# Optimization experiments

Measured on AMD Instinct MI355X. Metric: run time of the kernel, lower is better.

Reference implementation:

```python
import jax, jax.numpy as jnp
import numpy as np

B, D, N, M, H = 2, 256, 4096, 4096, 4
DIM = D // H          # per-head dim = 64
D8 = D // 8           # bottleneck = 32
TD = 2 * D            # concat channels = 512
TD8 = TD // 8         # mlp bottleneck = 64
BN_EPS = 1e-5


def _pw(x, W, b):
    # Conv1d kernel_size=1 == pointwise matmul over channel dim. x: [B,Cin,N]
    return jnp.einsum('oi,bin->bon', W, x) + b[None, :, None]


def setup_inputs() -> dict:
    key = jax.random.key(0)
    ks = jax.random.split(key, 32)
    s = 0.05
    p = lambda i, shape: jax.random.normal(ks[i], shape, dtype=jnp.float32) * s
    inp = {
        'x': jax.random.normal(ks[0], (B, D, N), dtype=jnp.float32),
        'source': jax.random.normal(ks[1], (B, D, M), dtype=jnp.float32),
        # proj[0] (query): Conv(D->D/8) then Conv(D/8->D)
        'Wq1': p(2, (D8, D)), 'bq1': p(3, (D8,)), 'Wq2': p(4, (D, D8)), 'bq2': p(5, (D,)),
        # proj[1] (key)
        'Wk1': p(6, (D8, D)), 'bk1': p(7, (D8,)), 'Wk2': p(8, (D, D8)), 'bk2': p(9, (D,)),
        # proj[2] (value)
        'Wv1': p(10, (D8, D)), 'bv1': p(11, (D8,)), 'Wv2': p(12, (D, D8)), 'bv2': p(13, (D,)),
        # merge
        'Wm1': p(14, (D8, D)), 'bm1': p(15, (D8,)), 'Wm2': p(16, (D, D8)), 'bm2': p(17, (D,)),
        # mlp: Conv(2D->2D/8), BN(gamma,beta), ReLU, Conv(2D/8->D) with zero-init bias
        'Wp1': p(18, (TD8, TD)), 'bp1': p(19, (TD8,)),
        'g1': jnp.ones((TD8,), dtype=jnp.float32) + p(20, (TD8,)),
        'be1': p(21, (TD8,)),
        'Wp2': p(22, (D, TD8)), 'bp2': jnp.zeros((D,), dtype=jnp.float32),
    }
    return inp


def reference(x, source, Wq1, bq1, Wq2, bq2, Wk1, bk1, Wk2, bk2, Wv1, bv1, Wv2, bv2,
              Wm1, bm1, Wm2, bm2, Wp1, bp1, g1, be1, Wp2, bp2):
    # bottleneck projections, then split channels into (per-head dim, heads)
    q = _pw(_pw(x, Wq1, bq1), Wq2, bq2).reshape(B, DIM, H, N)
    k = _pw(_pw(source, Wk1, bk1), Wk2, bk2).reshape(B, DIM, H, M)
    v = _pw(_pw(source, Wv1, bv1), Wv2, bv2).reshape(B, DIM, H, M)
    scores = jnp.einsum('bdhn,bdhm->bhnm', q, k) / jnp.sqrt(jnp.float32(DIM))
    prob = jax.nn.softmax(scores, axis=-1)          # [B,H,N,M] -- the big one
    msg = jnp.einsum('bhnm,bdhm->bdhn', prob, v).reshape(B, D, N)
    msg = _pw(_pw(msg, Wm1, bm1), Wm2, bm2)          # merge
    h = _pw(jnp.concatenate([x, msg], axis=1), Wp1, bp1)
    # BatchNorm1d in eval mode with running_mean=0, running_var=1
    h = jax.nn.relu(g1[None, :, None] * h / jnp.sqrt(1.0 + BN_EPS) + be1[None, :, None])
    return _pw(h, Wp2, bp2)
```

## Files before the change

kernel.cpp:

```cpp
#include <hip/hip_runtime.h>
#include <hip/hip_bf16.h>

typedef unsigned short ushort_t;
typedef unsigned int uint_t;

constexpr int Bb = 2, Dd = 256, Nn = 4096, Mm = 4096, Hh = 4;
constexpr int NSPLIT = 2;
constexpr int MCHUNK = Mm / NSPLIT;
constexpr int NT = MCHUNK / 64;
constexpr int BH = Bb * Hh;

typedef __attribute__((ext_vector_type(8))) short bf16x8;
typedef __attribute__((ext_vector_type(4))) float f32x4;

__device__ __forceinline__ ushort_t f2b(float f) {
    union { float f; uint_t u; } v; v.f = f;
    uint_t u = v.u;
    uint_t r = u + 0x7FFFu + ((u >> 16) & 1u);
    return (ushort_t)(r >> 16);
}

__device__ __forceinline__ int swz(int row, int ch, int rowlen, int keymask) {
    return row * rowlen + (((ch >> 3) ^ (row & keymask)) << 3) + (ch & 7);
}

__device__ __forceinline__ f32x4 MF(bf16x8 a, bf16x8 b, f32x4 c) {
    return __builtin_amdgcn_mfma_f32_16x16x32_bf16(a, b, c, 0, 0, 0);
}

#define BARRIER() do { __builtin_amdgcn_sched_barrier(0); __builtin_amdgcn_s_barrier(); __builtin_amdgcn_sched_barrier(0); } while (0)

__global__ __launch_bounds__(256) void cvt_weights(
    const float* __restrict__ Wq1, const float* __restrict__ Wq2,
    const float* __restrict__ Wk1, const float* __restrict__ Wk2,
    const float* __restrict__ Wv1, const float* __restrict__ Wv2,
    const float* __restrict__ Wm1, const float* __restrict__ Wm2,
    const float* __restrict__ Wp1, const float* __restrict__ Wp2,
    ushort_t* __restrict__ WB)
{
    const int i = blockIdx.x * 256 + threadIdx.x;
    const float* src; int off, n;
    switch (blockIdx.y) {
        case 0: src = Wq1; off = 0;     n = 8192;  break;
        case 1: src = Wq2; off = 8192;  n = 8192;  break;
        case 2: src = Wk1; off = 16384; n = 8192;  break;
        case 3: src = Wk2; off = 24576; n = 8192;  break;
        case 4: src = Wv1; off = 32768; n = 8192;  break;
        case 5: src = Wv2; off = 40960; n = 8192;  break;
        case 6: src = Wm1; off = 49152; n = 8192;  break;
        case 7: src = Wm2; off = 57344; n = 8192;  break;
        case 8: src = Wp1; off = 65536; n = 32768; break;
        default: src = Wp2; off = 98304; n = 16384; break;
    }
    if (i < n) WB[off + i] = f2b(src[i]);
}

__global__ __launch_bounds__(256) void proj_mfma(
    const float* __restrict__ x, const float* __restrict__ source,
    const ushort_t* __restrict__ WB,
    const float* __restrict__ bq1, const float* __restrict__ bq2,
    const float* __restrict__ bk1, const float* __restrict__ bk2,
    const float* __restrict__ bv1, const float* __restrict__ bv2,
    ushort_t* __restrict__ Qb, ushort_t* __restrict__ Kb, ushort_t* __restrict__ Vt)
{
    __shared__ __align__(16) ushort_t Xs[16 * 256];
    __shared__ __align__(16) ushort_t t1T[16 * 32];

    const int which = blockIdx.y;
    const float* X = (which == 0) ? x : source;
    const ushort_t* W1b = WB + which * 16384;
    const ushort_t* W2b = W1b + 8192;
    const float* b1 = (which == 0) ? bq1 : (which == 1) ? bk1 : bv1;
    const float* b2 = (which == 0) ? bq2 : (which == 1) ? bk2 : bv2;
    const float oscale = (which == 0) ? 0.125f * 1.44269504f : 1.0f;

    const int t = threadIdx.x;
    const int bpb = Nn / 16;
    const int b = blockIdx.x / bpb;
    const int n0 = (blockIdx.x % bpb) * 16;
    const int wave = t >> 6, lane = t & 63;
    const int r16 = lane & 15, q4 = lane >> 4;

    #pragma unroll
    for (int i = 0; i < 16; ++i) {
        int idx = t + i * 256;
        int c = idx >> 4, col = idx & 15;
        Xs[swz(col, c, 256, 7)] = f2b(X[(size_t)(b * Dd + c) * Nn + n0 + col]);
    }
    __syncthreads();

    if (wave < 2) {
        const int arow = wave * 16 + r16;
        const ushort_t* wrow = W1b + arow * 256;
        f32x4 acc = (f32x4){0.f, 0.f, 0.f, 0.f};
        #pragma unroll
        for (int kc = 0; kc < 8; ++kc) {
            bf16x8 af = *(const bf16x8*)(wrow + kc * 32 + q4 * 8);
            bf16x8 bfr = *(const bf16x8*)&Xs[swz(r16, kc * 32 + q4 * 8, 256, 7)];
            acc = MF(af, bfr, acc);
        }
        const int chb = wave * 16 + q4 * 4;
        ushort4 pk;
        pk.x = f2b(acc[0] + b1[chb + 0]);
        pk.y = f2b(acc[1] + b1[chb + 1]);
        pk.z = f2b(acc[2] + b1[chb + 2]);
        pk.w = f2b(acc[3] + b1[chb + 3]);
        *(ushort4*)&t1T[swz(r16, chb, 32, 3)] = pk;
    }
    __syncthreads();

    const bf16x8 bmid = *(const bf16x8*)&t1T[swz(r16, q4 * 8, 32, 3)];
    #pragma unroll
    for (int i = 0; i < 4; ++i) {
        const int rt = wave * 4 + i;
        const int arow = rt * 16 + r16;
        bf16x8 af = *(const bf16x8*)(W2b + arow * 32 + q4 * 8);
        f32x4 acc = MF(af, bmid, (f32x4){0.f, 0.f, 0.f, 0.f});
        const int chb = rt * 16 + q4 * 4;
        const int d = chb >> 2;
        if (which == 2) {
            #pragma unroll
            for (int r = 0; r < 4; ++r)
                Vt[(((size_t)(b * Hh + r)) * 64 + d) * (size_t)Nn + n0 + r16] =
                    f2b(acc[r] + b2[chb + r]);
        } else {
            ushort_t* O = (which == 0) ? Qb : Kb;
            #pragma unroll
            for (int r = 0; r < 4; ++r)
                O[(((size_t)(b * Hh + r)) * Nn + n0 + r16) * 64 + d] =
                    f2b((acc[r] + b2[chb + r]) * oscale);
        }
    }
}

__global__ __launch_bounds__(256, 4) void attn_kernel(
    const ushort_t* __restrict__ Qb, const ushort_t* __restrict__ Kb,
    const ushort_t* __restrict__ Vt,
    float* __restrict__ PO, float* __restrict__ PL)
{
    __shared__ __align__(16) ushort_t kvbuf[2][8192];
    __shared__ __align__(16) ushort_t plds[4][1024];

    const int bid0 = blockIdx.x;
    const int orig = (bid0 & 7) * 128 + (bid0 >> 3);
    const int nt_ = orig & 63;
    const int chunk = orig >> 6;
    const int sp = chunk & (NSPLIT - 1);
    const int bh = chunk >> 1;
    const int n0 = nt_ * 64;
    const int mbase = sp * MCHUNK;

    const int t = threadIdx.x;
    const int wave = t >> 6, lane = t & 63;
    const int r16 = lane & 15, q4 = lane >> 4;
    const int sw = r16 & 7;

    const ushort_t* qp = Qb + (((size_t)bh * Nn) + n0 + wave * 16 + r16) * 64 + q4 * 8;
    const bf16x8 aq0 = *(const bf16x8*)qp;
    const bf16x8 aq1 = *(const bf16x8*)(qp + 32);

    f32x4 accO[4];
    float lsum[4];
    #pragma unroll
    for (int i = 0; i < 4; ++i) { accO[i] = (f32x4){0.f, 0.f, 0.f, 0.f}; lsum[i] = 0.f; }

    const ushort_t* Ktile0 = Kb + ((size_t)bh * Mm + mbase) * 64;
    const ushort_t* Vrow0  = Vt + ((size_t)bh * 64) * (size_t)Mm + mbase;

    auto stage = [&](int buf, int kt) {
        const ushort_t* ks = Ktile0 + (size_t)kt * 64 * 64;
        const ushort_t* vs = Vrow0 + kt * 64;
        ushort_t* kb = &kvbuf[buf][0];
        ushort_t* vb = &kvbuf[buf][4096];
        #pragma unroll
        for (int p = 0; p < 2; ++p) {
            int c = p * 256 + t;
            int row = c >> 3, gs = (c & 7) ^ (row & 7);
            __builtin_amdgcn_global_load_lds((const uint_t*)(ks + row * 64 + gs * 8),
                                             (uint_t*)(kb + c * 8), 16, 0, 0);
        }
        #pragma unroll
        for (int p = 0; p < 2; ++p) {
            int c = p * 256 + t;
            int row = c >> 3, gs = (c & 7) ^ (row & 7);
            __builtin_amdgcn_global_load_lds((const uint_t*)(vs + (size_t)row * Mm + gs * 8),
                                             (uint_t*)(vb + c * 8), 16, 0, 0);
        }
    };

    stage(0, 0);
    int cur = 0;

    for (int kt = 0; kt < NT; ++kt) {
        if (kt + 1 < NT) {
            stage(cur ^ 1, kt + 1);
            asm volatile("s_waitcnt vmcnt(4)" ::: "memory");
        } else {
            asm volatile("s_waitcnt vmcnt(0)" ::: "memory");
        }
        BARRIER();

        const ushort_t* kb = &kvbuf[cur][0];
        const ushort_t* vb = &kvbuf[cur][4096];

        f32x4 s[4];
        #pragma unroll
        for (int mt = 0; mt < 4; ++mt) {
            int row = mt * 16 + r16;
            bf16x8 bk0 = *(const bf16x8*)(kb + row * 64 + ((q4 ^ sw) * 8));
            bf16x8 bk1 = *(const bf16x8*)(kb + row * 64 + (((q4 + 4) ^ sw) * 8));
            f32x4 a = (f32x4){0.f, 0.f, 0.f, 0.f};
            a = MF(aq0, bk0, a);
            a = MF(aq1, bk1, a);
            s[mt] = a;
        }

        ushort_t* pw = &plds[wave][0];
        #pragma unroll
        for (int r = 0; r < 4; ++r) {
            int prow = q4 * 4 + r;
            int rsw = prow & 7;
            #pragma unroll
            for (int mt = 0; mt < 4; ++mt) {
                float p = exp2f(s[mt][r]);
                lsum[r] += p;
                int pcol = mt * 16 + r16;
                pw[prow * 64 + (((pcol >> 3) ^ rsw) * 8) + (pcol & 7)] = f2b(p);
            }
        }
        bf16x8 ap0 = *(const bf16x8*)(pw + r16 * 64 + ((q4 ^ sw) * 8));
        bf16x8 ap1 = *(const bf16x8*)(pw + r16 * 64 + (((q4 + 4) ^ sw) * 8));

        #pragma unroll
        for (int dt = 0; dt < 4; ++dt) {
            int row = dt * 16 + r16;
            bf16x8 bv0 = *(const bf16x8*)(vb + row * 64 + ((q4 ^ sw) * 8));
            bf16x8 bv1 = *(const bf16x8*)(vb + row * 64 + (((q4 + 4) ^ sw) * 8));
            accO[dt] = MF(ap0, bv0, accO[dt]);
            accO[dt] = MF(ap1, bv1, accO[dt]);
        }
        BARRIER();
        cur ^= 1;
    }

    const size_t pobase = ((size_t)sp * BH + bh) * Nn;
    #pragma unroll
    for (int r = 0; r < 4; ++r) {
        float rs = lsum[r];
        rs += __shfl_xor(rs, 1);
        rs += __shfl_xor(rs, 2);
        rs += __shfl_xor(rs, 4);
        rs += __shfl_xor(rs, 8);
        lsum[r] = rs;
    }
    #pragma unroll
    for (int dt = 0; dt < 4; ++dt) {
        #pragma unroll
        for (int r = 0; r < 4; ++r) {
            int n = n0 + wave * 16 + q4 * 4 + r;
            PO[(pobase + n) * 64 + dt * 16 + r16] = accO[dt][r];
        }
    }
    if (r16 == 0) {
        #pragma unroll
        for (int r = 0; r < 4; ++r) {
            int n = n0 + wave * 16 + q4 * 4 + r;
            PL[pobase + n] = lsum[r];
        }
    }
}

__global__ __launch_bounds__(256) void tail_mfma(
    const float* __restrict__ X,
    const float* __restrict__ PO, const float* __restrict__ PL,
    const ushort_t* __restrict__ WB,
    const float* __restrict__ bm1, const float* __restrict__ bm2,
    const float* __restrict__ bp1,
    const float* __restrict__ G1, const float* __restrict__ BE1,
    const float* __restrict__ bp2,
    float* __restrict__ out)
{
    const ushort_t* Wm1b = WB + 49152;
    const ushort_t* Wm2b = WB + 57344;
    const ushort_t* Wp1b = WB + 65536;
    const ushort_t* Wp2b = WB + 98304;

    __shared__ __align__(16) ushort_t msgT[16 * 256];
    __shared__ __align__(16) ushort_t catT[16 * 512];
    __shared__ __align__(16) ushort_t t1T[16 * 32];
    __shared__ __align__(16) ushort_t hT[16 * 64];
    __shared__ float inv[4][16];

    const int t = threadIdx.x;
    const int bpb = Nn / 16;
    const int b = blockIdx.x / bpb;
    const int n0 = (blockIdx.x % bpb) * 16;
    const int wave = t >> 6, lane = t & 63;
    const int r16 = lane & 15, q4 = lane >> 4;

    if (t < 64) {
        const int h = t >> 4, nn = t & 15;
        const size_t ro = ((size_t)(b * Hh + h)) * Nn + n0 + nn;
        const size_t so = (size_t)BH * Nn;
        float den = 0.f;
        #pragma unroll
        for (int sp = 0; sp < NSPLIT; ++sp) den += PL[sp * so + ro];
        inv[h][nn] = 1.0f / den;
    }
    #pragma unroll
    for (int i = 0; i < 16; ++i) {
        int idx = t + i * 256;
        int c = idx >> 4, col = idx & 15;
        catT[swz(col, c, 512, 7)] = f2b(X[(size_t)(b * Dd + c) * Nn + n0 + col]);
    }
    __syncthreads();

    {
        const size_t so64 = (size_t)BH * Nn * 64;
        #pragma unroll
        for (int i = 0; i < 16; ++i) {
            int idx = t + i * 256;
            int d = idx & 63, h = (idx >> 6) & 3, nn = idx >> 8;
            size_t base = (((size_t)(b * Hh + h) * Nn) + n0 + nn) * 64 + d;
            float a = (PO[base] + PO[so64 + base]) * inv[h][nn];
            msgT[swz(nn, d * 4 + h, 256, 7)] = f2b(a);
        }
    }
    __syncthreads();

    if (wave < 2) {
        const int arow = wave * 16 + r16;
        const ushort_t* wrow = Wm1b + arow * 256;
        f32x4 acc = (f32x4){0.f, 0.f, 0.f, 0.f};
        #pragma unroll
        for (int kc = 0; kc < 8; ++kc) {
            bf16x8 af = *(const bf16x8*)(wrow + kc * 32 + q4 * 8);
            bf16x8 bfr = *(const bf16x8*)&msgT[swz(r16, kc * 32 + q4 * 8, 256, 7)];
            acc = MF(af, bfr, acc);
        }
        const int chb = wave * 16 + q4 * 4;
        ushort4 pk;
        pk.x = f2b(acc[0] + bm1[chb + 0]);
        pk.y = f2b(acc[1] + bm1[chb + 1]);
        pk.z = f2b(acc[2] + bm1[chb + 2]);
        pk.w = f2b(acc[3] + bm1[chb + 3]);
        *(ushort4*)&t1T[swz(r16, chb, 32, 3)] = pk;
    }
    __syncthreads();

    {
        const bf16x8 bt1 = *(const bf16x8*)&t1T[swz(r16, q4 * 8, 32, 3)];
        #pragma unroll
        for (int i = 0; i < 4; ++i) {
            const int rt = wave * 4 + i;
            const int arow = rt * 16 + r16;
            bf16x8 af = *(const bf16x8*)(Wm2b + arow * 32 + q4 * 8);
            f32x4 acc = MF(af, bt1, (f32x4){0.f, 0.f, 0.f, 0.f});
            const int chb = rt * 16 + q4 * 4;
            ushort4 pk;
            pk.x = f2b(acc[0] + bm2[chb + 0]);
            pk.y = f2b(acc[1] + bm2[chb + 1]);
            pk.z = f2b(acc[2] + bm2[chb + 2]);
            pk.w = f2b(acc[3] + bm2[chb + 3]);
            *(ushort4*)&catT[swz(r16, 256 + chb, 512, 7)] = pk;
        }
    }
    __syncthreads();

    {
        const int arow = wave * 16 + r16;
        const ushort_t* wrow = Wp1b + arow * 512;
        f32x4 acc = (f32x4){0.f, 0.f, 0.f, 0.f};
        #pragma unroll
        for (int kc = 0; kc < 16; ++kc) {
            bf16x8 af = *(const bf16x8*)(wrow + kc * 32 + q4 * 8);
            bf16x8 bfr = *(const bf16x8*)&catT[swz(r16, kc * 32 + q4 * 8, 512, 7)];
            acc = MF(af, bfr, acc);
        }
        const float bnscale = rsqrtf(1.0f + 1e-5f);
        const int chb = wave * 16 + q4 * 4;
        ushort4 pk;
        ushort_t* pp = (ushort_t*)&pk;
        #pragma unroll
        for (int r = 0; r < 4; ++r) {
            int ch = chb + r;
            float v = fmaxf(0.f, G1[ch] * (acc[r] + bp1[ch]) * bnscale + BE1[ch]);
            pp[r] = f2b(v);
        }
        *(ushort4*)&hT[swz(r16, chb, 64, 7)] = pk;
    }
    __syncthreads();

    {
        const bf16x8 bh0 = *(const bf16x8*)&hT[swz(r16, q4 * 8, 64, 7)];
        const bf16x8 bh1 = *(const bf16x8*)&hT[swz(r16, 32 + q4 * 8, 64, 7)];
        #pragma unroll
        for (int i = 0; i < 4; ++i) {
            const int rt = wave * 4 + i;
            const int arow = rt * 16 + r16;
            bf16x8 af0 = *(const bf16x8*)(Wp2b + arow * 64 + q4 * 8);
            bf16x8 af1 = *(const bf16x8*)(Wp2b + arow * 64 + 32 + q4 * 8);
            f32x4 acc = MF(af0, bh0, (f32x4){0.f, 0.f, 0.f, 0.f});
            acc = MF(af1, bh1, acc);
            const int chb = rt * 16 + q4 * 4;
            #pragma unroll
            for (int r = 0; r < 4; ++r)
                out[(size_t)(b * Dd + chb + r) * Nn + n0 + r16] = acc[r] + bp2[chb + r];
        }
    }
}

extern "C" void kernel_launch(void* const* d_in, const int* in_sizes, int n_in,
                              void* d_out, int out_size, void* d_ws, size_t ws_size,
                              hipStream_t stream)
{
    const float* x      = (const float*)d_in[0];
    const float* source = (const float*)d_in[1];
    const float* Wq1 = (const float*)d_in[2];  const float* bq1 = (const float*)d_in[3];
    const float* Wq2 = (const float*)d_in[4];  const float* bq2 = (const float*)d_in[5];
    const float* Wk1 = (const float*)d_in[6];  const float* bk1 = (const float*)d_in[7];
    const float* Wk2 = (const float*)d_in[8];  const float* bk2 = (const float*)d_in[9];
    const float* Wv1 = (const float*)d_in[10]; const float* bv1 = (const float*)d_in[11];
    const float* Wv2 = (const float*)d_in[12]; const float* bv2 = (const float*)d_in[13];
    const float* Wm1 = (const float*)d_in[14]; const float* bm1 = (const float*)d_in[15];
    const float* Wm2 = (const float*)d_in[16]; const float* bm2 = (const float*)d_in[17];
    const float* Wp1 = (const float*)d_in[18]; const float* bp1 = (const float*)d_in[19];
    const float* g1  = (const float*)d_in[20]; const float* be1 = (const float*)d_in[21];
    const float* Wp2 = (const float*)d_in[22]; const float* bp2 = (const float*)d_in[23];

    ushort_t* Qb = (ushort_t*)d_ws;
    ushort_t* Kb = Qb + (size_t)BH * Nn * 64;
    ushort_t* Vt = Kb + (size_t)BH * Mm * 64;
    float*    PO = (float*)(Vt + (size_t)BH * 64 * Mm);
    float*    PL = PO + (size_t)NSPLIT * BH * Nn * 64;
    ushort_t* WB = (ushort_t*)(PL + (size_t)NSPLIT * BH * Nn);

    cvt_weights<<<dim3(128, 10), 256, 0, stream>>>(
        Wq1, Wq2, Wk1, Wk2, Wv1, Wv2, Wm1, Wm2, Wp1, Wp2, WB);

    proj_mfma<<<dim3(Bb * Nn / 16, 3), 256, 0, stream>>>(
        x, source, WB, bq1, bq2, bk1, bk2, bv1, bv2, Qb, Kb, Vt);

    attn_kernel<<<BH * NSPLIT * (Nn / 64), 256, 0, stream>>>(Qb, Kb, Vt, PO, PL);

    tail_mfma<<<Bb * Nn / 16, 256, 0, stream>>>(x, PO, PL, WB,
                                                bm1, bm2, bp1, g1, be1, bp2,
                                                (float*)d_out);
}
```

Baseline: 210.3 us.

## Keep P in registers, double query rows per wave, permute V columns

Each attention wave now handles two 16-row query tiles, so every K/V fragment read from shared memory is used twice. The score MFMA is transposed so the exponentiated probabilities already sit in the A-operand layout. They are packed with v_cvt_pk_bf16_f32 and fed straight into the PV MFMA, which removes the per-wave P round-trip through shared memory. To make this valid, the projection kernel writes V columns in a permuted order, and Q/K are staged through shared memory for coalesced 16-byte stores. The cost is more registers per thread (occupancy hint lowered from 4 to 2) and half as many attention blocks.

```diff
diff --git a/kernel.cpp b/kernel.cpp
--- a/kernel.cpp
+++ b/kernel.cpp
@@ -12,12 +12,19 @@
 
 typedef __attribute__((ext_vector_type(8))) short bf16x8;
 typedef __attribute__((ext_vector_type(4))) float f32x4;
+typedef __attribute__((ext_vector_type(4))) uint_t u32x4;
 
 __device__ __forceinline__ ushort_t f2b(float f) {
     union { float f; uint_t u; } v; v.f = f;
     uint_t u = v.u;
     uint_t r = u + 0x7FFFu + ((u >> 16) & 1u);
     return (ushort_t)(r >> 16);
+}
+
+__device__ __forceinline__ uint_t pk2(float lo, float hi) {
+    uint_t r;
+    asm("v_cvt_pk_bf16_f32 %0, %1, %2" : "=v"(r) : "v"(lo), "v"(hi));
+    return r;
 }
 
 __device__ __forceinline__ int swz(int row, int ch, int rowlen, int keymask) {
@@ -65,6 +72,7 @@
 {
     __shared__ __align__(16) ushort_t Xs[16 * 256];
     __shared__ __align__(16) ushort_t t1T[16 * 32];
+    __shared__ __align__(16) ushort_t oT[4 * 16 * 72];
 
     const int which = blockIdx.y;
     const float* X = (which == 0) ? x : source;
@@ -110,44 +118,64 @@
     __syncthreads();
 
     const bf16x8 bmid = *(const bf16x8*)&t1T[swz(r16, q4 * 8, 32, 3)];
-    #pragma unroll
-    for (int i = 0; i < 4; ++i) {
-        const int rt = wave * 4 + i;
-        const int arow = rt * 16 + r16;
-        bf16x8 af = *(const bf16x8*)(W2b + arow * 32 + q4 * 8);
-        f32x4 acc = MF(af, bmid, (f32x4){0.f, 0.f, 0.f, 0.f});
-        const int chb = rt * 16 + q4 * 4;
-        const int d = chb >> 2;
-        if (which == 2) {
+    if (which == 2) {
+        const int a = (n0 >> 4) & 3;
+        const int kp = ((a >> 1) * 32) + ((r16 >> 2) * 8) + ((a & 1) * 4) + (r16 & 3);
+        const int colbase = n0 & ~63;
+        #pragma unroll
+        for (int i = 0; i < 4; ++i) {
+            const int rt = wave * 4 + i;
+            bf16x8 af = *(const bf16x8*)(W2b + (rt * 16 + r16) * 32 + q4 * 8);
+            f32x4 acc = MF(af, bmid, (f32x4){0.f, 0.f, 0.f, 0.f});
+            const int chb = rt * 16 + q4 * 4;
+            const int d = chb >> 2;
             #pragma unroll
             for (int r = 0; r < 4; ++r)
-                Vt[(((size_t)(b * Hh + r)) * 64 + d) * (size_t)Nn + n0 + r16] =
+                Vt[(((size_t)(b * Hh + r)) * 64 + d) * (size_t)Nn + colbase + kp] =
                     f2b(acc[r] + b2[chb + r]);
-        } else {
-            ushort_t* O = (which == 0) ? Qb : Kb;
+        }
+    } else {
+        #pragma unroll
+        for (int i = 0; i < 4; ++i) {
+            const int rt = wave * 4 + i;
+            bf16x8 af = *(const bf16x8*)(W2b + (rt * 16 + r16) * 32 + q4 * 8);
+            f32x4 acc = MF(af, bmid, (f32x4){0.f, 0.f, 0.f, 0.f});
+            const int chb = rt * 16 + q4 * 4;
+            const int d = chb >> 2;
+            const int dg = d >> 3, de = d & 7;
             #pragma unroll
-            for (int r = 0; r < 4; ++r)
-                O[(((size_t)(b * Hh + r)) * Nn + n0 + r16) * 64 + d] =
-                    f2b((acc[r] + b2[chb + r]) * oscale);
-        }
-    }
-}
-
-__global__ __launch_bounds__(256, 4) void attn_kernel(
+            for (int r = 0; r < 4; ++r) {
+                float v = (acc[r] + b2[chb + r]) * oscale;
+                oT[(r * 16 + r16) * 72 + ((dg ^ (r16 & 7)) << 3) + de] = f2b(v);
+            }
+        }
+        __syncthreads();
+        ushort_t* O = (which == 0) ? Qb : Kb;
+        #pragma unroll
+        for (int k = 0; k < 2; ++k) {
+            int c = t + k * 256;
+            int row = c >> 3, dg2 = c & 7;
+            int h = row >> 4, n = row & 15;
+            bf16x8 v = *(const bf16x8*)&oT[row * 72 + ((dg2 ^ (n & 7)) << 3)];
+            *(bf16x8*)&O[(((size_t)(b * Hh + h)) * Nn + n0 + n) * 64 + dg2 * 8] = v;
+        }
+    }
+}
+
+__global__ __launch_bounds__(256, 2) void attn_kernel(
     const ushort_t* __restrict__ Qb, const ushort_t* __restrict__ Kb,
     const ushort_t* __restrict__ Vt,
     float* __restrict__ PO, float* __restrict__ PL)
 {
     __shared__ __align__(16) ushort_t kvbuf[2][8192];
-    __shared__ __align__(16) ushort_t plds[4][1024];
 
     const int bid0 = blockIdx.x;
-    const int orig = (bid0 & 7) * 128 + (bid0 >> 3);
-    const int nt_ = orig & 63;
-    const int chunk = orig >> 6;
+    const int orig = (bid0 & 7) * 64 + (bid0 >> 3);
+    const int nt_ = orig & 31;
+    const int chunk = orig >> 5;
     const int sp = chunk & (NSPLIT - 1);
     const int bh = chunk >> 1;
-    const int n0 = nt_ * 64;
+    const int n0 = nt_ * 128;
     const int mbase = sp * MCHUNK;
 
     const int t = threadIdx.x;
@@ -155,14 +183,19 @@
     const int r16 = lane & 15, q4 = lane >> 4;
     const int sw = r16 & 7;
 
-    const ushort_t* qp = Qb + (((size_t)bh * Nn) + n0 + wave * 16 + r16) * 64 + q4 * 8;
-    const bf16x8 aq0 = *(const bf16x8*)qp;
-    const bf16x8 aq1 = *(const bf16x8*)(qp + 32);
-
-    f32x4 accO[4];
-    float lsum[4];
+    const ushort_t* qp = Qb + (((size_t)bh * Nn) + n0 + wave * 32 + r16) * 64 + q4 * 8;
+    const bf16x8 aq00 = *(const bf16x8*)qp;
+    const bf16x8 aq01 = *(const bf16x8*)(qp + 32);
+    const bf16x8 aq10 = *(const bf16x8*)(qp + 16 * 64);
+    const bf16x8 aq11 = *(const bf16x8*)(qp + 16 * 64 + 32);
+
+    f32x4 accO0[4], accO1[4];
+    float lsum0 = 0.f, lsum1 = 0.f;
     #pragma unroll
-    for (int i = 0; i < 4; ++i) { accO[i] = (f32x4){0.f, 0.f, 0.f, 0.f}; lsum[i] = 0.f; }
+    for (int i = 0; i < 4; ++i) {
+        accO0[i] = (f32x4){0.f, 0.f, 0.f, 0.f};
+        accO1[i] = (f32x4){0.f, 0.f, 0.f, 0.f};
+    }
 
     const ushort_t* Ktile0 = Kb + ((size_t)bh * Mm + mbase) * 64;
     const ushort_t* Vrow0  = Vt + ((size_t)bh * 64) * (size_t)Mm + mbase;
@@ -203,70 +236,72 @@
         const ushort_t* kb = &kvbuf[cur][0];
         const ushort_t* vb = &kvbuf[cur][4096];
 
-        f32x4 s[4];
+        f32x4 s0[4], s1[4];
         #pragma unroll
         for (int mt = 0; mt < 4; ++mt) {
             int row = mt * 16 + r16;
             bf16x8 bk0 = *(const bf16x8*)(kb + row * 64 + ((q4 ^ sw) * 8));
             bf16x8 bk1 = *(const bf16x8*)(kb + row * 64 + (((q4 + 4) ^ sw) * 8));
-            f32x4 a = (f32x4){0.f, 0.f, 0.f, 0.f};
-            a = MF(aq0, bk0, a);
-            a = MF(aq1, bk1, a);
-            s[mt] = a;
-        }
-
-        ushort_t* pw = &plds[wave][0];
-        #pragma unroll
-        for (int r = 0; r < 4; ++r) {
-            int prow = q4 * 4 + r;
-            int rsw = prow & 7;
+            f32x4 a0 = MF(bk0, aq00, (f32x4){0.f, 0.f, 0.f, 0.f});
+            s0[mt] = MF(bk1, aq01, a0);
+            f32x4 a1 = MF(bk0, aq10, (f32x4){0.f, 0.f, 0.f, 0.f});
+            s1[mt] = MF(bk1, aq11, a1);
+        }
+
+        #pragma unroll
+        for (int mt = 0; mt < 4; ++mt) {
             #pragma unroll
-            for (int mt = 0; mt < 4; ++mt) {
-                float p = exp2f(s[mt][r]);
-                lsum[r] += p;
-                int pcol = mt * 16 + r16;
-                pw[prow * 64 + (((pcol >> 3) ^ rsw) * 8) + (pcol & 7)] = f2b(p);
+            for (int r = 0; r < 4; ++r) {
+                float p0 = exp2f(s0[mt][r]); lsum0 += p0; s0[mt][r] = p0;
+                float p1 = exp2f(s1[mt][r]); lsum1 += p1; s1[mt][r] = p1;
             }
         }
-        bf16x8 ap0 = *(const bf16x8*)(pw + r16 * 64 + ((q4 ^ sw) * 8));
-        bf16x8 ap1 = *(const bf16x8*)(pw + r16 * 64 + (((q4 + 4) ^ sw) * 8));
+        u32x4 u;
+        u.x = pk2(s0[0][0], s0[0][1]); u.y = pk2(s0[0][2], s0[0][3]);
+        u.z = pk2(s0[1][0], s0[1][1]); u.w = pk2(s0[1][2], s0[1][3]);
+        bf16x8 ap00 = __builtin_bit_cast(bf16x8, u);
+        u.x = pk2(s0[2][0], s0[2][1]); u.y = pk2(s0[2][2], s0[2][3]);
+        u.z = pk2(s0[3][0], s0[3][1]); u.w = pk2(s0[3][2], s0[3][3]);
+        bf16x8 ap01 = __builtin_bit_cast(bf16x8, u);
+        u.x = pk2(s1[0][0], s1[0][1]); u.y = pk2(s1[0][2], s1[0][3]);
+        u.z = pk2(s1[1][0], s1[1][1]); u.w = pk2(s1[1][2], s1[1][3]);
+        bf16x8 ap10 = __builtin_bit_cast(bf16x8, u);
+        u.x = pk2(s1[2][0], s1[2][1]); u.y = pk2(s1[2][2], s1[2][3]);
+        u.z = pk2(s1[3][0], s1[3][1]); u.w = pk2(s1[3][2], s1[3][3]);
+        bf16x8 ap11 = __builtin_bit_cast(bf16x8, u);
 
         #pragma unroll
         for (int dt = 0; dt < 4; ++dt) {
             int row = dt * 16 + r16;
             bf16x8 bv0 = *(const bf16x8*)(vb + row * 64 + ((q4 ^ sw) * 8));
             bf16x8 bv1 = *(const bf16x8*)(vb + row * 64 + (((q4 + 4) ^ sw) * 8));
-            accO[dt] = MF(ap0, bv0, accO[dt]);
-            accO[dt] = MF(ap1, bv1, accO[dt]);
+            accO0[dt] = MF(ap00, bv0, accO0[dt]);
+            accO0[dt] = MF(ap01, bv1, accO0[dt]);
+            accO1[dt] = MF(ap10, bv0, accO1[dt]);
+            accO1[dt] = MF(ap11, bv1, accO1[dt]);
         }
         BARRIER();
         cur ^= 1;
     }
 
+    lsum0 += __shfl_xor(lsum0, 16);
+    lsum0 += __shfl_xor(lsum0, 32);
+    lsum1 += __shfl_xor(lsum1, 16);
+    lsum1 += __shfl_xor(lsum1, 32);
+
     const size_t pobase = ((size_t)sp * BH + bh) * Nn;
     #pragma unroll
-    for (int r = 0; r < 4; ++r) {
-        float rs = lsum[r];
-        rs += __shfl_xor(rs, 1);
-        rs += __shfl_xor(rs, 2);
-        rs += __shfl_xor(rs, 4);
-        rs += __shfl_xor(rs, 8);
-        lsum[r] = rs;
-    }
-    #pragma unroll
     for (int dt = 0; dt < 4; ++dt) {
         #pragma unroll
         for (int r = 0; r < 4; ++r) {
-            int n = n0 + wave * 16 + q4 * 4 + r;
-            PO[(pobase + n) * 64 + dt * 16 + r16] = accO[dt][r];
-        }
-    }
-    if (r16 == 0) {
-        #pragma unroll
-        for (int r = 0; r < 4; ++r) {
-            int n = n0 + wave * 16 + q4 * 4 + r;
-            PL[pobase + n] = lsum[r];
-        }
+            int nA = n0 + wave * 32 + q4 * 4 + r;
+            PO[(pobase + nA) * 64 + dt * 16 + r16] = accO0[dt][r];
+            PO[(pobase + nA + 16) * 64 + dt * 16 + r16] = accO1[dt][r];
+        }
+    }
+    if (q4 == 0) {
+        PL[pobase + n0 + wave * 32 + r16] = lsum0;
+        PL[pobase + n0 + wave * 32 + 16 + r16] = lsum1;
     }
 }
 
@@ -353,8 +388,7 @@
         #pragma unroll
         for (int i = 0; i < 4; ++i) {
             const int rt = wave * 4 + i;
-            const int arow = rt * 16 + r16;
-            bf16x8 af = *(const bf16x8*)(Wm2b + arow * 32 + q4 * 8);
+            bf16x8 af = *(const bf16x8*)(Wm2b + (rt * 16 + r16) * 32 + q4 * 8);
             f32x4 acc = MF(af, bt1, (f32x4){0.f, 0.f, 0.f, 0.f});
             const int chb = rt * 16 + q4 * 4;
             ushort4 pk;
@@ -397,9 +431,8 @@
         #pragma unroll
         for (int i = 0; i < 4; ++i) {
             const int rt = wave * 4 + i;
-            const int arow = rt * 16 + r16;
-            bf16x8 af0 = *(const bf16x8*)(Wp2b + arow * 64 + q4 * 8);
-            bf16x8 af1 = *(const bf16x8*)(Wp2b + arow * 64 + 32 + q4 * 8);
+            bf16x8 af0 = *(const bf16x8*)(Wp2b + (rt * 16 + r16) * 64 + q4 * 8);
+            bf16x8 af1 = *(const bf16x8*)(Wp2b + (rt * 16 + r16) * 64 + 32 + q4 * 8);
             f32x4 acc = MF(af0, bh0, (f32x4){0.f, 0.f, 0.f, 0.f});
             acc = MF(af1, bh1, acc);
             const int chb = rt * 16 + q4 * 4;
@@ -441,7 +474,7 @@
     proj_mfma<<<dim3(Bb * Nn / 16, 3), 256, 0, stream>>>(
         x, source, WB, bq1, bq2, bk1, bk2, bv1, bv2, Qb, Kb, Vt);
 
-    attn_kernel<<<BH * NSPLIT * (Nn / 64), 256, 0, stream>>>(Qb, Kb, Vt, PO, PL);
+    attn_kernel<<<BH * NSPLIT * (Nn / 128), 256, 0, stream>>>(Qb, Kb, Vt, PO, PL);
 
     tail_mfma<<<Bb * Nn / 16, 256, 0, stream>>>(x, PO, PL, WB,
                                                 bm1, bm2, bp1, g1, be1, bp2,
```

Measured after the change: 188.0 us. 1.12x faster.
